# Kernel tuning notes

Measured on AMD Instinct MI355X. Metric: run time of the kernel, lower is better.

Reference implementation:

```python
import jax, jax.numpy as jnp
import numpy as np
from jax import lax

KERNEL_SIZE = 3
THRE_TIMES = 5.0
THRE_POINT = 1000.0


def _coeff_matrix(H, W, dtype):
    k = KERNEL_SIZE
    c_edge = k / (k // 2 + 1)              # 1.5 for k=3
    c_corner = (k * k) / (k // 2 + 1) ** 2  # 2.25 for k=3
    coeff = jnp.ones((H, W), dtype)
    coeff = coeff.at[0, :].set(c_edge).at[-1, :].set(c_edge)
    coeff = coeff.at[:, 0].set(c_edge).at[:, -1].set(c_edge)
    coeff = coeff.at[0, 0].set(c_corner).at[0, -1].set(c_corner)
    coeff = coeff.at[-1, 0].set(c_corner).at[-1, -1].set(c_corner)
    return coeff


def _box_filter(img):
    # cv2.filter2D with borderType=0 == zero-padded SAME convolution
    k = KERNEL_SIZE
    kern = jnp.full((1, 1, k, k), 1.0 / (k * k), img.dtype)
    x = img[None, None]  # NCHW
    y = lax.conv_general_dilated(x, kern, window_strides=(1, 1), padding='SAME')
    return y[0, 0]


def _neighbor_sum_count(img):
    H, W = img.shape
    zr = jnp.zeros((1, W), img.dtype)
    zc = jnp.zeros((H, 1), img.dtype)
    up = jnp.concatenate([zr, img[:-1]], axis=0)      # img[x-1, y]
    down = jnp.concatenate([img[1:], zr], axis=0)     # img[x+1, y]
    left = jnp.concatenate([zc, img[:, :-1]], axis=1) # img[x, y-1]
    right = jnp.concatenate([img[:, 1:], zc], axis=1) # img[x, y+1]
    nsum = up + down + left + right
    r = jnp.arange(H)
    c = jnp.arange(W)
    cnt = ((r > 0).astype(img.dtype) + (r < H - 1).astype(img.dtype))[:, None] \
        + ((c > 0).astype(img.dtype) + (c < W - 1).astype(img.dtype))[None, :]
    return nsum, cnt


def setup_inputs() -> dict:
    key = jax.random.key(0)
    img = jax.random.normal(key, (8192, 8192), dtype=jnp.float32)
    return {"img": img}


def reference(img) -> jnp.ndarray:
    H, W = img.shape
    # CheckBadPoint
    img_mean = _box_filter(img) * _coeff_matrix(H, W, img.dtype)
    mask = (img > THRE_TIMES * img_mean) | (img > THRE_POINT)
    # neighbor-average repair (ele_sum // num -> floor division)
    nsum, cnt = _neighbor_sum_count(img)
    repaired = jnp.floor(nsum / cnt)
    return jnp.where(mask, repaired, img)
```

## Files before the change

### kernel.cpp

```cpp
#include <hip/hip_runtime.h>
#include <math.h>

#define IMG_H 8192
#define IMG_W 8192

__global__ __launch_bounds__(256) void repair_kernel(const float* __restrict__ img,
                                                     float* __restrict__ out) {
    const int x4 = (blockIdx.x * blockDim.x + threadIdx.x) * 4;
    const int y  = blockIdx.y * blockDim.y + threadIdx.y;

    const float inv9 = 1.0f / 9.0f;

    float v[3][6];
    #pragma unroll
    for (int r = 0; r < 3; ++r) {
        const int yy = y + r - 1;
        const bool row_valid = (yy >= 0) && (yy < IMG_H);
        if (row_valid) {
            const float* rowp = img + (size_t)yy * IMG_W;
            const float4 c = *(const float4*)(rowp + x4);
            v[r][1] = c.x; v[r][2] = c.y; v[r][3] = c.z; v[r][4] = c.w;
            v[r][0] = (x4 > 0)         ? rowp[x4 - 1] : 0.0f;
            v[r][5] = (x4 + 4 < IMG_W) ? rowp[x4 + 4] : 0.0f;
        } else {
            #pragma unroll
            for (int j = 0; j < 6; ++j) v[r][j] = 0.0f;
        }
    }

    const bool row_edge = (y == 0) || (y == IMG_H - 1);
    const float cnt_row = (float)((y > 0) + (y < IMG_H - 1));

    float res[4];
    #pragma unroll
    for (int j = 0; j < 4; ++j) {
        const int gx = x4 + j;
        const float x = v[1][j + 1];

        float acc = 0.0f;
        #pragma unroll
        for (int r = 0; r < 3; ++r) {
            #pragma unroll
            for (int c = 0; c < 3; ++c) {
                acc = __fadd_rn(acc, __fmul_rn(v[r][j + c], inv9));
            }
        }

        const bool col_edge = (gx == 0) || (gx == IMG_W - 1);
        const float coeff = (row_edge && col_edge) ? 2.25f
                          : ((row_edge || col_edge) ? 1.5f : 1.0f);
        const float img_mean = __fmul_rn(acc, coeff);

        const bool mask = (x > __fmul_rn(5.0f, img_mean)) || (x > 1000.0f);

        const float up    = v[0][j + 1];
        const float down  = v[2][j + 1];
        const float left  = v[1][j];
        const float right = v[1][j + 2];
        const float nsum  = __fadd_rn(__fadd_rn(__fadd_rn(up, down), left), right);

        const float cnt = cnt_row + (float)((gx > 0) + (gx < IMG_W - 1));
        const float repaired = floorf(__fdiv_rn(nsum, cnt));

        res[j] = mask ? repaired : x;
    }

    float4 o;
    o.x = res[0]; o.y = res[1]; o.z = res[2]; o.w = res[3];
    *(float4*)(out + (size_t)y * IMG_W + x4) = o;
}

extern "C" void kernel_launch(void* const* d_in, const int* in_sizes, int n_in,
                              void* d_out, int out_size, void* d_ws, size_t ws_size,
                              hipStream_t stream) {
    const float* img = (const float*)d_in[0];
    float* out = (float*)d_out;

    dim3 block(64, 4);
    dim3 grid(IMG_W / (64 * 4), IMG_H / 4);
    repair_kernel<<<grid, block, 0, stream>>>(img, out);
}
```

Before: 485.4 us.

## Process two rows per thread with branch-free interior fast path and nontemporal stores

```diff
diff --git a/kernel.cpp b/kernel.cpp
--- a/kernel.cpp
+++ b/kernel.cpp
@@ -4,70 +4,116 @@
 #define IMG_H 8192
 #define IMG_W 8192
 
+typedef float vfloat4 __attribute__((ext_vector_type(4)));
+
 __global__ __launch_bounds__(256) void repair_kernel(const float* __restrict__ img,
                                                      float* __restrict__ out) {
-    const int x4 = (blockIdx.x * blockDim.x + threadIdx.x) * 4;
-    const int y  = blockIdx.y * blockDim.y + threadIdx.y;
+    const int bx = blockIdx.x, by = blockIdx.y;
+    const int x4 = (bx * 64 + threadIdx.x) * 4;
+    const int y0 = (by * 4 + threadIdx.y) * 2;
 
     const float inv9 = 1.0f / 9.0f;
 
-    float v[3][6];
-    #pragma unroll
-    for (int r = 0; r < 3; ++r) {
-        const int yy = y + r - 1;
-        const bool row_valid = (yy >= 0) && (yy < IMG_H);
-        if (row_valid) {
-            const float* rowp = img + (size_t)yy * IMG_W;
-            const float4 c = *(const float4*)(rowp + x4);
+    const bool interior = (bx > 0) & (bx < (int)gridDim.x - 1) &
+                          (by > 0) & (by < (int)gridDim.y - 1);
+
+    if (interior) {
+        float v[4][6];
+        const float* p = img + (size_t)(y0 - 1) * IMG_W + x4;
+        #pragma unroll
+        for (int r = 0; r < 4; ++r) {
+            const float4 c = *(const float4*)p;
+            v[r][0] = p[-1];
             v[r][1] = c.x; v[r][2] = c.y; v[r][3] = c.z; v[r][4] = c.w;
-            v[r][0] = (x4 > 0)         ? rowp[x4 - 1] : 0.0f;
-            v[r][5] = (x4 + 4 < IMG_W) ? rowp[x4 + 4] : 0.0f;
-        } else {
+            v[r][5] = p[4];
+            p += IMG_W;
+        }
+
+        #pragma unroll
+        for (int r = 0; r < 2; ++r) {
+            float res[4];
             #pragma unroll
-            for (int j = 0; j < 6; ++j) v[r][j] = 0.0f;
+            for (int j = 0; j < 4; ++j) {
+                float acc = 0.0f;
+                #pragma unroll
+                for (int rr = 0; rr < 3; ++rr)
+                    #pragma unroll
+                    for (int cc = 0; cc < 3; ++cc)
+                        acc = __fadd_rn(acc, __fmul_rn(v[r + rr][j + cc], inv9));
+
+                const float x = v[r + 1][j + 1];
+                const bool mask = (x > __fmul_rn(5.0f, acc)) || (x > 1000.0f);
+
+                const float nsum = __fadd_rn(
+                    __fadd_rn(__fadd_rn(v[r][j + 1], v[r + 2][j + 1]), v[r + 1][j]),
+                    v[r + 1][j + 2]);
+                const float rep = floorf(__fmul_rn(nsum, 0.25f));
+
+                res[j] = mask ? rep : x;
+            }
+            vfloat4 o;
+            o.x = res[0]; o.y = res[1]; o.z = res[2]; o.w = res[3];
+            __builtin_nontemporal_store(o, (vfloat4*)(out + (size_t)(y0 + r) * IMG_W + x4));
+        }
+    } else {
+        #pragma unroll
+        for (int r = 0; r < 2; ++r) {
+            const int y = y0 + r;
+
+            float v[3][6];
+            #pragma unroll
+            for (int rr = 0; rr < 3; ++rr) {
+                const int yy = y + rr - 1;
+                const bool row_valid = (yy >= 0) && (yy < IMG_H);
+                if (row_valid) {
+                    const float* rowp = img + (size_t)yy * IMG_W;
+                    const float4 c = *(const float4*)(rowp + x4);
+                    v[rr][1] = c.x; v[rr][2] = c.y; v[rr][3] = c.z; v[rr][4] = c.w;
+                    v[rr][0] = (x4 > 0)         ? rowp[x4 - 1] : 0.0f;
+                    v[rr][5] = (x4 + 4 < IMG_W) ? rowp[x4 + 4] : 0.0f;
+                } else {
+                    #pragma unroll
+                    for (int j = 0; j < 6; ++j) v[rr][j] = 0.0f;
+                }
+            }
+
+            const bool row_edge = (y == 0) || (y == IMG_H - 1);
+            const float cnt_row = (float)((y > 0) + (y < IMG_H - 1));
+
+            float res[4];
+            #pragma unroll
+            for (int j = 0; j < 4; ++j) {
+                const int gx = x4 + j;
+                const float x = v[1][j + 1];
+
+                float acc = 0.0f;
+                #pragma unroll
+                for (int rr = 0; rr < 3; ++rr)
+                    #pragma unroll
+                    for (int cc = 0; cc < 3; ++cc)
+                        acc = __fadd_rn(acc, __fmul_rn(v[rr][j + cc], inv9));
+
+                const bool col_edge = (gx == 0) || (gx == IMG_W - 1);
+                const float coeff = (row_edge && col_edge) ? 2.25f
+                                  : ((row_edge || col_edge) ? 1.5f : 1.0f);
+                const float img_mean = __fmul_rn(acc, coeff);
+
+                const bool mask = (x > __fmul_rn(5.0f, img_mean)) || (x > 1000.0f);
+
+                const float nsum = __fadd_rn(
+                    __fadd_rn(__fadd_rn(v[0][j + 1], v[2][j + 1]), v[1][j]),
+                    v[1][j + 2]);
+
+                const float cnt = cnt_row + (float)((gx > 0) + (gx < IMG_W - 1));
+                const float rep = floorf(__fdiv_rn(nsum, cnt));
+
+                res[j] = mask ? rep : x;
+            }
+            float4 o;
+            o.x = res[0]; o.y = res[1]; o.z = res[2]; o.w = res[3];
+            *(float4*)(out + (size_t)y * IMG_W + x4) = o;
         }
     }
-
-    const bool row_edge = (y == 0) || (y == IMG_H - 1);
-    const float cnt_row = (float)((y > 0) + (y < IMG_H - 1));
-
-    float res[4];
-    #pragma unroll
-    for (int j = 0; j < 4; ++j) {
-        const int gx = x4 + j;
-        const float x = v[1][j + 1];
-
-        float acc = 0.0f;
-        #pragma unroll
-        for (int r = 0; r < 3; ++r) {
-            #pragma unroll
-            for (int c = 0; c < 3; ++c) {
-                acc = __fadd_rn(acc, __fmul_rn(v[r][j + c], inv9));
-            }
-        }
-
-        const bool col_edge = (gx == 0) || (gx == IMG_W - 1);
-        const float coeff = (row_edge && col_edge) ? 2.25f
-                          : ((row_edge || col_edge) ? 1.5f : 1.0f);
-        const float img_mean = __fmul_rn(acc, coeff);
-
-        const bool mask = (x > __fmul_rn(5.0f, img_mean)) || (x > 1000.0f);
-
-        const float up    = v[0][j + 1];
-        const float down  = v[2][j + 1];
-        const float left  = v[1][j];
-        const float right = v[1][j + 2];
-        const float nsum  = __fadd_rn(__fadd_rn(__fadd_rn(up, down), left), right);
-
-        const float cnt = cnt_row + (float)((gx > 0) + (gx < IMG_W - 1));
-        const float repaired = floorf(__fdiv_rn(nsum, cnt));
-
-        res[j] = mask ? repaired : x;
-    }
-
-    float4 o;
-    o.x = res[0]; o.y = res[1]; o.z = res[2]; o.w = res[3];
-    *(float4*)(out + (size_t)y * IMG_W + x4) = o;
 }
 
 extern "C" void kernel_launch(void* const* d_in, const int* in_sizes, int n_in,
@@ -77,6 +123,6 @@
     float* out = (float*)d_out;
 
     dim3 block(64, 4);
-    dim3 grid(IMG_W / (64 * 4), IMG_H / 4);
+    dim3 grid(IMG_W / 256, IMG_H / 8);
     repair_kernel<<<grid, block, 0, stream>>>(img, out);
 }
```

After: 480.5 us. No clear change (-1.0%).

## Process 8 rows per thread with rolling row window and shuffle halos

Applied to the files above, without the earlier changes.

```diff
diff --git a/kernel.cpp b/kernel.cpp
--- a/kernel.cpp
+++ b/kernel.cpp
@@ -3,71 +3,99 @@
 
 #define IMG_H 8192
 #define IMG_W 8192
+#define ROWS_PER_THREAD 8
+
+typedef float vfloat4 __attribute__((ext_vector_type(4)));
 
 __global__ __launch_bounds__(256) void repair_kernel(const float* __restrict__ img,
                                                      float* __restrict__ out) {
-    const int x4 = (blockIdx.x * blockDim.x + threadIdx.x) * 4;
-    const int y  = blockIdx.y * blockDim.y + threadIdx.y;
+    const int bx = blockIdx.x;
+    const int lane = threadIdx.x;
+    const int x4 = bx * 256 + lane * 4;
+    const int y0 = (blockIdx.y * blockDim.y + threadIdx.y) * ROWS_PER_THREAD;
+    const bool x_edge_blk = (bx == 0) || (bx == (int)gridDim.x - 1);
 
     const float inv9 = 1.0f / 9.0f;
 
-    float v[3][6];
+    float w[3][6];
+
+    auto load_row = [&](int yy, float* row) {
+        if (yy >= 0 && yy < IMG_H) {
+            const float* rp = img + (size_t)yy * IMG_W + x4;
+            const float4 c = *(const float4*)rp;
+            float lw = __shfl_up(c.w, 1);
+            float rw = __shfl_down(c.x, 1);
+            if (lane == 0)  lw = (x4 > 0)         ? rp[-1] : 0.0f;
+            if (lane == 63) rw = (x4 + 4 < IMG_W) ? rp[4]  : 0.0f;
+            row[0] = lw; row[1] = c.x; row[2] = c.y; row[3] = c.z; row[4] = c.w; row[5] = rw;
+        } else {
+            row[0] = row[1] = row[2] = row[3] = row[4] = row[5] = 0.0f;
+        }
+    };
+
+    load_row(y0 - 1, w[0]);
+    load_row(y0,     w[1]);
+
     #pragma unroll
-    for (int r = 0; r < 3; ++r) {
-        const int yy = y + r - 1;
-        const bool row_valid = (yy >= 0) && (yy < IMG_H);
-        if (row_valid) {
-            const float* rowp = img + (size_t)yy * IMG_W;
-            const float4 c = *(const float4*)(rowp + x4);
-            v[r][1] = c.x; v[r][2] = c.y; v[r][3] = c.z; v[r][4] = c.w;
-            v[r][0] = (x4 > 0)         ? rowp[x4 - 1] : 0.0f;
-            v[r][5] = (x4 + 4 < IMG_W) ? rowp[x4 + 4] : 0.0f;
-        } else {
+    for (int r = 0; r < ROWS_PER_THREAD; ++r) {
+        load_row(y0 + r + 1, w[(r + 2) % 3]);
+        const float* up  = w[r % 3];
+        const float* mid = w[(r + 1) % 3];
+        const float* dn  = w[(r + 2) % 3];
+        const int y = y0 + r;
+
+        float res[4];
+        #pragma unroll
+        for (int j = 0; j < 4; ++j) {
+            float acc = 0.0f;
             #pragma unroll
-            for (int j = 0; j < 6; ++j) v[r][j] = 0.0f;
+            for (int cc = 0; cc < 3; ++cc) acc = __fadd_rn(acc, __fmul_rn(up[j + cc],  inv9));
+            #pragma unroll
+            for (int cc = 0; cc < 3; ++cc) acc = __fadd_rn(acc, __fmul_rn(mid[j + cc], inv9));
+            #pragma unroll
+            for (int cc = 0; cc < 3; ++cc) acc = __fadd_rn(acc, __fmul_rn(dn[j + cc],  inv9));
+
+            const float x = mid[j + 1];
+            const bool mask = (x > __fmul_rn(5.0f, acc)) || (x > 1000.0f);
+            const float nsum = __fadd_rn(
+                __fadd_rn(__fadd_rn(up[j + 1], dn[j + 1]), mid[j]), mid[j + 2]);
+            const float rep = floorf(__fmul_rn(nsum, 0.25f));
+            res[j] = mask ? rep : x;
         }
-    }
 
-    const bool row_edge = (y == 0) || (y == IMG_H - 1);
-    const float cnt_row = (float)((y > 0) + (y < IMG_H - 1));
+        const bool row_edge = (y == 0) || (y == IMG_H - 1);
+        if (x_edge_blk || row_edge) {
+            const float cnt_row = (float)((y > 0) + (y < IMG_H - 1));
+            #pragma unroll
+            for (int j = 0; j < 4; ++j) {
+                const int gx = x4 + j;
+                const bool col_edge = (gx == 0) || (gx == IMG_W - 1);
+                if (col_edge || row_edge) {
+                    float acc = 0.0f;
+                    #pragma unroll
+                    for (int cc = 0; cc < 3; ++cc) acc = __fadd_rn(acc, __fmul_rn(up[j + cc],  inv9));
+                    #pragma unroll
+                    for (int cc = 0; cc < 3; ++cc) acc = __fadd_rn(acc, __fmul_rn(mid[j + cc], inv9));
+                    #pragma unroll
+                    for (int cc = 0; cc < 3; ++cc) acc = __fadd_rn(acc, __fmul_rn(dn[j + cc],  inv9));
 
-    float res[4];
-    #pragma unroll
-    for (int j = 0; j < 4; ++j) {
-        const int gx = x4 + j;
-        const float x = v[1][j + 1];
-
-        float acc = 0.0f;
-        #pragma unroll
-        for (int r = 0; r < 3; ++r) {
-            #pragma unroll
-            for (int c = 0; c < 3; ++c) {
-                acc = __fadd_rn(acc, __fmul_rn(v[r][j + c], inv9));
+                    const float coeff = (row_edge && col_edge) ? 2.25f : 1.5f;
+                    const float img_mean = __fmul_rn(acc, coeff);
+                    const float x = mid[j + 1];
+                    const bool mask = (x > __fmul_rn(5.0f, img_mean)) || (x > 1000.0f);
+                    const float nsum = __fadd_rn(
+                        __fadd_rn(__fadd_rn(up[j + 1], dn[j + 1]), mid[j]), mid[j + 2]);
+                    const float cnt = cnt_row + (float)((gx > 0) + (gx < IMG_W - 1));
+                    const float rep = floorf(__fdiv_rn(nsum, cnt));
+                    res[j] = mask ? rep : x;
+                }
             }
         }
 
-        const bool col_edge = (gx == 0) || (gx == IMG_W - 1);
-        const float coeff = (row_edge && col_edge) ? 2.25f
-                          : ((row_edge || col_edge) ? 1.5f : 1.0f);
-        const float img_mean = __fmul_rn(acc, coeff);
-
-        const bool mask = (x > __fmul_rn(5.0f, img_mean)) || (x > 1000.0f);
-
-        const float up    = v[0][j + 1];
-        const float down  = v[2][j + 1];
-        const float left  = v[1][j];
-        const float right = v[1][j + 2];
-        const float nsum  = __fadd_rn(__fadd_rn(__fadd_rn(up, down), left), right);
-
-        const float cnt = cnt_row + (float)((gx > 0) + (gx < IMG_W - 1));
-        const float repaired = floorf(__fdiv_rn(nsum, cnt));
-
-        res[j] = mask ? repaired : x;
+        vfloat4 o;
+        o.x = res[0]; o.y = res[1]; o.z = res[2]; o.w = res[3];
+        __builtin_nontemporal_store(o, (vfloat4*)(out + (size_t)y * IMG_W + x4));
     }
-
-    float4 o;
-    o.x = res[0]; o.y = res[1]; o.z = res[2]; o.w = res[3];
-    *(float4*)(out + (size_t)y * IMG_W + x4) = o;
 }
 
 extern "C" void kernel_launch(void* const* d_in, const int* in_sizes, int n_in,
@@ -77,6 +105,6 @@
     float* out = (float*)d_out;
 
     dim3 block(64, 4);
-    dim3 grid(IMG_W / (64 * 4), IMG_H / 4);
+    dim3 grid(IMG_W / 256, IMG_H / (4 * ROWS_PER_THREAD));
     repair_kernel<<<grid, block, 0, stream>>>(img, out);
 }
```

After: 449.2 us. -7.4%, faster.
